# Optimization experiments

Measured on AMD Instinct MI355X. Metric: run time of the kernel, lower is better.

Reference implementation:

```python
import jax, jax.numpy as jnp
import numpy as np

N_NODES = 100000
N_EDGES = 1600000
HIDDEN = 128
N_REL = 8


def setup_inputs() -> dict:
    key = jax.random.key(0)
    ks = jax.random.split(key, 12)
    s = 1.0 / np.sqrt(HIDDEN)
    inp = {
        "node_idx": jnp.arange(N_NODES, dtype=jnp.int32),
        "edge_index": jax.random.randint(ks[0], (2, N_EDGES), 0, N_NODES, dtype=jnp.int32),
        "edge_type": jax.random.randint(ks[1], (N_EDGES,), 0, N_REL, dtype=jnp.int32),
        "embedding": jax.random.normal(ks[2], (N_NODES, HIDDEN), jnp.float32),
        "W_rel_0": jax.random.normal(ks[3], (N_REL, HIDDEN, HIDDEN), jnp.float32) * s,
        "W_root_0": jax.random.normal(ks[4], (HIDDEN, HIDDEN), jnp.float32) * s,
        "b_0": jnp.zeros((HIDDEN,), jnp.float32),
        "W_rel_1": jax.random.normal(ks[5], (N_REL, HIDDEN, HIDDEN), jnp.float32) * s,
        "W_root_1": jax.random.normal(ks[6], (HIDDEN, HIDDEN), jnp.float32) * s,
        "b_1": jnp.zeros((HIDDEN,), jnp.float32),
    }
    return inp


def _rgcn_conv(x, src, dst, et, W_rel, W_root, b):
    # PyG RGCNConv: out_i = x_i @ W_root + b + sum_r mean_{j in N_r(i)} x_j @ W_r
    n = x.shape[0]
    r = W_rel.shape[0]
    # Transform all nodes by all relations once (R small), then gather per edge.
    x_all = jnp.einsum('nd,rdf->rnf', x, W_rel)          # [R, N, d]
    msg = x_all[et, src]                                  # [E, d]
    # per-(relation, dst) mean normalization
    seg = et * n + dst                                    # [E]
    deg = jax.ops.segment_sum(jnp.ones(et.shape, jnp.float32), seg, num_segments=r * n)
    norm = 1.0 / jnp.maximum(deg[seg], 1.0)               # [E]
    agg = jax.ops.segment_sum(msg * norm[:, None], dst, num_segments=n)  # [N, d]
    return agg + x @ W_root + b


def reference(node_idx, edge_index, edge_type, embedding,
              W_rel_0, W_root_0, b_0, W_rel_1, W_root_1, b_1):
    src, dst = edge_index[0], edge_index[1]
    x = embedding[node_idx]
    x = jax.nn.relu(_rgcn_conv(x, src, dst, edge_type, W_rel_0, W_root_0, b_0))
    x = jax.nn.relu(_rgcn_conv(x, src, dst, edge_type, W_rel_1, W_root_1, b_1))
    return x
```

## Files before the change

### kernel.cpp

```cpp
#include <hip/hip_runtime.h>
#include <hip/hip_bf16.h>

typedef short bf16x8 __attribute__((ext_vector_type(8)));
typedef float f32x4 __attribute__((ext_vector_type(4)));

constexpr int NN = 100000;
constexpr int NE = 1600000;
constexpr int HH = 128;
constexpr int NR = 8;
constexpr int NBIN = 782;
constexpr int CAPB = 6144;

__device__ __forceinline__ unsigned short f2bf(float f) {
    unsigned b = __float_as_uint(f);
    b += 0x7fffu + ((b >> 16) & 1u);
    return (unsigned short)(b >> 16);
}

__global__ void convertWX(const float* __restrict__ Wr0, const float* __restrict__ Wq0,
                          const float* __restrict__ Wr1, const float* __restrict__ Wq1,
                          unsigned short* __restrict__ Wt,
                          const int* __restrict__ node_idx,
                          const float* __restrict__ emb,
                          unsigned* __restrict__ xb32) {
    if (blockIdx.x < 1152) {
        int o = blockIdx.x * 256 + threadIdx.x;
        int L = o / 147456;
        int rem = o - L * 147456;
        int s = rem >> 14;
        int p = rem & 16383;
        int f = p >> 7;
        int d = p & 127;
        const float* Wq = L ? Wq1 : Wq0;
        const float* Wr = L ? Wr1 : Wr0;
        float v = (s == 0) ? Wq[d * 128 + f] : Wr[((s - 1) * 128 + d) * 128 + f];
        Wt[o] = f2bf(v);
    } else {
        int i = (blockIdx.x - 1152) * 256 + threadIdx.x;
        if (i >= NN * 64) return;
        int n = i >> 6, dp = i & 63;
        int row = node_idx[n];
        float2 v = *((const float2*)(emb + (size_t)row * HH) + dp);
        xb32[(size_t)n * 64 + dp] = (unsigned)f2bf(v.x) | ((unsigned)f2bf(v.y) << 16);
    }
}

__global__ __launch_bounds__(256) void binCount(const int* __restrict__ edst,
                                                unsigned* __restrict__ binCounts) {
    __shared__ unsigned hist[NBIN];
    for (int i = threadIdx.x; i < NBIN; i += 256) hist[i] = 0;
    __syncthreads();
    int stride = gridDim.x * 256;
    for (int e = blockIdx.x * 256 + threadIdx.x; e < NE; e += stride)
        atomicAdd(&hist[((unsigned)edst[e]) >> 7], 1u);
    __syncthreads();
    for (int i = threadIdx.x; i < NBIN; i += 256)
        if (hist[i]) atomicAdd(&binCounts[i], hist[i]);
}

__global__ void binScan(const unsigned* __restrict__ binCounts,
                        unsigned* __restrict__ binStarts,
                        unsigned* __restrict__ binCursor) {
    __shared__ unsigned sh[1024];
    int tid = threadIdx.x;
    unsigned v = (tid < NBIN) ? binCounts[tid] : 0u;
    sh[tid] = v;
    __syncthreads();
    for (int ofs = 1; ofs < 1024; ofs <<= 1) {
        unsigned t = (tid >= ofs) ? sh[tid - ofs] : 0u;
        __syncthreads();
        sh[tid] += t;
        __syncthreads();
    }
    if (tid < NBIN) {
        unsigned s = sh[tid] - v;
        binStarts[tid] = s;
        binCursor[tid] = s;
    }
    if (tid == 0) binStarts[NBIN] = NE;
}

__global__ __launch_bounds__(256) void binScatter(
        const int* __restrict__ esrc, const int* __restrict__ edst,
        const int* __restrict__ etype, unsigned* __restrict__ binCursor,
        unsigned* __restrict__ binned) {
    __shared__ unsigned hist[NBIN];
    __shared__ unsigned cur[NBIN];
    for (int i = threadIdx.x; i < NBIN; i += 256) hist[i] = 0;
    __syncthreads();
    int per = (NE + gridDim.x - 1) / gridDim.x;
    int lo = blockIdx.x * per;
    int hi = lo + per; if (hi > NE) hi = NE;
    for (int e = lo + threadIdx.x; e < hi; e += 256)
        atomicAdd(&hist[((unsigned)edst[e]) >> 7], 1u);
    __syncthreads();
    for (int i = threadIdx.x; i < NBIN; i += 256) {
        unsigned c = hist[i];
        cur[i] = c ? atomicAdd(&binCursor[i], c) : 0u;
    }
    __syncthreads();
    for (int e = lo + threadIdx.x; e < hi; e += 256) {
        unsigned d = (unsigned)edst[e];
        unsigned b = d >> 7;
        unsigned pos = atomicAdd(&cur[b], 1u);
        binned[pos] = (unsigned)esrc[e] | (((unsigned)etype[e]) << 17) |
                      ((d & 127u) << 20);
    }
}

__global__ __launch_bounds__(256) void binSort(
        const unsigned* __restrict__ binStarts, const unsigned* __restrict__ binned,
        unsigned* __restrict__ epk, unsigned* __restrict__ starts) {
    __shared__ unsigned hist[1024];
    __shared__ unsigned scn[1024];
    __shared__ unsigned cnts[1024];
    __shared__ unsigned part[256];
    __shared__ unsigned buf[CAPB];
    __shared__ unsigned outb[CAPB];
    int bin = blockIdx.x;
    int tid = threadIdx.x;
    unsigned base = binStarts[bin];
    int cnt = (int)(binStarts[bin + 1] - base);

    for (int i = tid; i < 1024; i += 256) hist[i] = 0;
    __syncthreads();
    for (int i = tid; i < cnt; i += 256) {
        unsigned p = binned[base + i];
        if (i < CAPB) buf[i] = p;
        atomicAdd(&hist[(p >> 17) & 0x3ffu], 1u);
    }
    __syncthreads();
    unsigned h4[4], tsum = 0;
#pragma unroll
    for (int j = 0; j < 4; ++j) { h4[j] = hist[tid * 4 + j]; tsum += h4[j]; }
    part[tid] = tsum;
    __syncthreads();
    for (int ofs = 1; ofs < 256; ofs <<= 1) {
        unsigned t = (tid >= ofs) ? part[tid - ofs] : 0u;
        __syncthreads();
        part[tid] += t;
        __syncthreads();
    }
    unsigned run = part[tid] - tsum;
#pragma unroll
    for (int j = 0; j < 4; ++j) { scn[tid * 4 + j] = run; run += h4[j]; }
    __syncthreads();
    for (int i = tid; i < 1024; i += 256) {
        starts[(size_t)bin * 1024 + i] = base + scn[i];
        cnts[i] = hist[i];
        hist[i] = scn[i];
    }
    __syncthreads();
    if (cnt <= CAPB) {
        for (int i = tid; i < cnt; i += 256) {
            unsigned p = buf[i];
            unsigned key = (p >> 17) & 0x3ffu;
            unsigned pos = atomicAdd(&hist[key], 1u);
            unsigned deg = cnts[key]; if (deg > 4095u) deg = 4095u;
            outb[pos] = ((p & 0x1ffffu) << 3) | (key & 7u) | (deg << 20);
        }
        __syncthreads();
        for (int i = tid; i < cnt; i += 256) epk[base + i] = outb[i];
    } else {
        for (int i = tid; i < cnt; i += 256) {
            unsigned p = binned[base + i];
            unsigned key = (p >> 17) & 0x3ffu;
            unsigned pos = atomicAdd(&hist[key], 1u);
            unsigned deg = cnts[key]; if (deg > 4095u) deg = 4095u;
            epk[base + pos] = ((p & 0x1ffffu) << 3) | (key & 7u) | (deg << 20);
        }
    }
}

__global__ __launch_bounds__(256) void bigGemm(const unsigned short* x,
                                               const unsigned short* __restrict__ Wt,
                                               unsigned* __restrict__ y32,
                                               unsigned* root32) {
    constexpr int LDA = 136;
    __shared__ __align__(16) unsigned short A_lds[64 * LDA];
    __shared__ __align__(16) unsigned short B_lds[128 * LDA];

    int tid = threadIdx.x;
    int wid = tid >> 6, lane = tid & 63;
    int quad = lane >> 4, l16 = lane & 15;
    int wr = wid >> 1, wc = wid & 1;
    int m0 = blockIdx.x * 64;
    int chunk = tid & 15, rip = tid >> 4;

#pragma unroll
    for (int p = 0; p < 4; ++p) {
        int r = p * 16 + rip;
        int node = m0 + r;
        node = node < NN ? node : NN - 1;
        uint4 v = *((const uint4*)(x + (size_t)node * HH) + chunk);
        *(uint4*)(&A_lds[r * LDA + chunk * 8]) = v;
    }

    for (int s = 0; s < 9; ++s) {
        __syncthreads();
#pragma unroll
        for (int p = 0; p < 8; ++p) {
            int r = p * 16 + rip;
            uint4 v = *((const uint4*)(Wt + s * 16384 + r * 128) + chunk);
            *(uint4*)(&B_lds[r * LDA + chunk * 8]) = v;
        }
        __syncthreads();

        f32x4 acc[2][4];
#pragma unroll
        for (int nt = 0; nt < 2; ++nt)
#pragma unroll
            for (int ft = 0; ft < 4; ++ft) acc[nt][ft] = (f32x4){0.f, 0.f, 0.f, 0.f};

#pragma unroll
        for (int kt = 0; kt < 4; ++kt) {
            int ko = kt * 32 + quad * 8;
            bf16x8 aW[4], bx[2];
#pragma unroll
            for (int ft = 0; ft < 4; ++ft)
                aW[ft] = *(const bf16x8*)(&B_lds[(wc * 64 + ft * 16 + l16) * LDA + ko]);
#pragma unroll
            for (int nt = 0; nt < 2; ++nt)
                bx[nt] = *(const bf16x8*)(&A_lds[(wr * 32 + nt * 16 + l16) * LDA + ko]);
#pragma unroll
            for (int nt = 0; nt < 2; ++nt)
#pragma unroll
                for (int ft = 0; ft < 4; ++ft)
                    acc[nt][ft] = __builtin_amdgcn_mfma_f32_16x16x32_bf16(
                        aW[ft], bx[nt], acc[nt][ft], 0, 0, 0);
        }
#pragma unroll
        for (int nt = 0; nt < 2; ++nt) {
            int node = m0 + wr * 32 + nt * 16 + l16;
            if (node < NN) {
                unsigned* dst = (s == 0) ? (root32 + (size_t)node * 64)
                                         : (y32 + ((size_t)node * 8 + (s - 1)) * 64);
#pragma unroll
                for (int ft = 0; ft < 4; ++ft) {
                    int f0 = wc * 64 + ft * 16 + quad * 4;
                    unsigned d0, d1;
                    asm("v_cvt_pk_bf16_f32 %0, %1, %2"
                        : "=v"(d0) : "v"(acc[nt][ft][0]), "v"(acc[nt][ft][1]));
                    asm("v_cvt_pk_bf16_f32 %0, %1, %2"
                        : "=v"(d1) : "v"(acc[nt][ft][2]), "v"(acc[nt][ft][3]));
                    *(uint2*)(dst + (f0 >> 1)) = make_uint2(d0, d1);
                }
            }
        }
    }
}

__global__ __launch_bounds__(256) void scatterAgg(
        const unsigned* __restrict__ starts, const unsigned* __restrict__ epk,
        const unsigned* __restrict__ y32, const unsigned* root32,
        const float* __restrict__ bias,
        float* __restrict__ outF, unsigned* outB) {
    int node = blockIdx.x * 4 + (threadIdx.x >> 6);
    if (node >= NN) return;
    int lane = threadIdx.x & 63;

    unsigned s0 = starts[(size_t)node * 8];
    unsigned s1 = starts[(size_t)node * 8 + 8];
    int cnt = (int)__builtin_amdgcn_readfirstlane((int)(s1 - s0));

    float ax = 0.f, ay = 0.f;
    for (int c0 = 0; c0 < cnt; c0 += 64) {
        unsigned myE = s0 + (unsigned)c0 + (unsigned)lane;
        unsigned pk = (myE < s1) ? epk[myE] : 0u;
        float nrm = __builtin_amdgcn_rcpf((float)(pk >> 20));
        int cend = cnt - c0;
        if (cend > 64) cend = 64;
        for (int base = 0; base < cend; base += 8) {
            int m = cend - base;
            if (m > 8) m = 8;
            int bix = base << 2;
            unsigned pj[8], qj[8];
            float nj[8];
#pragma unroll
            for (int j = 0; j < 8; ++j) {
                pj[j] = (unsigned)__builtin_amdgcn_ds_bpermute(bix + (j << 2), (int)pk);
                nj[j] = __uint_as_float(
                    (unsigned)__builtin_amdgcn_ds_bpermute(bix + (j << 2),
                                                           __float_as_int(nrm)));
            }
#pragma unroll
            for (int j = 0; j < 8; ++j)
                if (j < m) qj[j] = y32[((pj[j] & 0xFFFFFu) << 6) + (unsigned)lane];
#pragma unroll
            for (int j = 0; j < 8; ++j) {
                if (j < m) {
                    float lo = __uint_as_float(qj[j] << 16);
                    float hi = __uint_as_float(qj[j] & 0xffff0000u);
                    ax += lo * nj[j];
                    ay += hi * nj[j];
                }
            }
        }
    }

    unsigned r = root32[(size_t)node * 64 + lane];
    float2 bv = ((const float2*)bias)[lane];
    float ox = ax + __uint_as_float(r << 16) + bv.x;
    float oy = ay + __uint_as_float(r & 0xffff0000u) + bv.y;
    ox = ox > 0.f ? ox : 0.f;
    oy = oy > 0.f ? oy : 0.f;
    if (outF) {
        *(float2*)(outF + (size_t)node * HH + lane * 2) = make_float2(ox, oy);
    } else {
        outB[(size_t)node * 64 + lane] =
            (unsigned)f2bf(ox) | ((unsigned)f2bf(oy) << 16);
    }
}

extern "C" void kernel_launch(void* const* d_in, const int* in_sizes, int n_in,
                              void* d_out, int out_size, void* d_ws, size_t ws_size,
                              hipStream_t stream) {
    const int* node_idx = (const int*)d_in[0];
    const int* eidx     = (const int*)d_in[1];
    const int* etype    = (const int*)d_in[2];
    const float* emb    = (const float*)d_in[3];
    const float* Wr0    = (const float*)d_in[4];
    const float* Wq0    = (const float*)d_in[5];
    const float* b0     = (const float*)d_in[6];
    const float* Wr1    = (const float*)d_in[7];
    const float* Wq1    = (const float*)d_in[8];
    const float* b1     = (const float*)d_in[9];
    const int* esrc = eidx;
    const int* edst = eidx + NE;

    char* ws = (char*)d_ws;
    size_t off = 0;
    auto alloc = [&](size_t bytes) -> void* {
        void* p = ws + off;
        off = (off + bytes + 255) & ~(size_t)255;
        return p;
    };
    unsigned* binCounts = (unsigned*)alloc((size_t)NBIN * 4);
    unsigned* binStarts = (unsigned*)alloc((size_t)(NBIN + 1) * 4);
    unsigned* binCursor = (unsigned*)alloc((size_t)NBIN * 4);
    unsigned* starts    = (unsigned*)alloc((size_t)NBIN * 1024 * 4);
    unsigned* epk       = (unsigned*)alloc((size_t)NE * 4);
    unsigned* xb32      = (unsigned*)alloc((size_t)NN * 64 * 4);
    unsigned* y32       = (unsigned*)alloc((size_t)NN * 8 * 64 * 4);
    unsigned short* Wt  = (unsigned short*)alloc((size_t)2 * 9 * 16384 * 2);
    unsigned* binned = y32;
    (void)ws_size; (void)n_in; (void)in_sizes; (void)out_size;

    hipMemsetAsync(binCounts, 0, (size_t)NBIN * 4, stream);
    convertWX<<<1152 + (NN * 64 + 255) / 256, 256, 0, stream>>>(
        Wr0, Wq0, Wr1, Wq1, Wt, node_idx, emb, xb32);
    binCount<<<256, 256, 0, stream>>>(edst, binCounts);
    binScan<<<1, 1024, 0, stream>>>(binCounts, binStarts, binCursor);
    binScatter<<<128, 256, 0, stream>>>(esrc, edst, etype, binCursor, binned);
    binSort<<<NBIN, 256, 0, stream>>>(binStarts, binned, epk, starts);

    int nblk = (NN + 63) / 64;
    bigGemm<<<nblk, 256, 0, stream>>>((const unsigned short*)xb32, Wt, y32, xb32);
    scatterAgg<<<(NN + 3) / 4, 256, 0, stream>>>(starts, epk, y32, xb32, b0,
                                                 nullptr, xb32);
    bigGemm<<<nblk, 256, 0, stream>>>((const unsigned short*)xb32, Wt + 147456,
                                      y32, xb32);
    scatterAgg<<<(NN + 3) / 4, 256, 0, stream>>>(starts, epk, y32, xb32, b1,
                                                 (float*)d_out, nullptr);
}
```

Before: 552.9 us.

## Load GEMM operands directly into registers, dropping LDS staging

The bigGemm kernel no longer stages the node tile and weight tiles through shared memory. Each wave loads its x fragments into registers once and reloads weight fragments per relation straight from global memory (relying on cache), which removes the LDS copies and the two barriers per stage. Launch bounds now request 3 blocks per CU. In exchange, register pressure rises and weight reads become redundant across waves and blocks, served by L1/L2 rather than LDS.

```diff
diff --git a/kernel.cpp b/kernel.cpp
--- a/kernel.cpp
+++ b/kernel.cpp
@@ -172,39 +172,36 @@
     }
 }
 
-__global__ __launch_bounds__(256) void bigGemm(const unsigned short* x,
-                                               const unsigned short* __restrict__ Wt,
-                                               unsigned* __restrict__ y32,
-                                               unsigned* root32) {
-    constexpr int LDA = 136;
-    __shared__ __align__(16) unsigned short A_lds[64 * LDA];
-    __shared__ __align__(16) unsigned short B_lds[128 * LDA];
-
+__global__ __launch_bounds__(256, 3) void bigGemm(const unsigned short* x,
+                                                  const unsigned short* __restrict__ Wt,
+                                                  unsigned* __restrict__ y32,
+                                                  unsigned* root32) {
     int tid = threadIdx.x;
     int wid = tid >> 6, lane = tid & 63;
     int quad = lane >> 4, l16 = lane & 15;
     int wr = wid >> 1, wc = wid & 1;
     int m0 = blockIdx.x * 64;
-    int chunk = tid & 15, rip = tid >> 4;
-
-#pragma unroll
-    for (int p = 0; p < 4; ++p) {
-        int r = p * 16 + rip;
-        int node = m0 + r;
+
+    bf16x8 ax[2][4];
+#pragma unroll
+    for (int nt = 0; nt < 2; ++nt) {
+        int node = m0 + wr * 32 + nt * 16 + l16;
         node = node < NN ? node : NN - 1;
-        uint4 v = *((const uint4*)(x + (size_t)node * HH) + chunk);
-        *(uint4*)(&A_lds[r * LDA + chunk * 8]) = v;
-    }
+        const unsigned short* rp = x + (size_t)node * HH + quad * 8;
+#pragma unroll
+        for (int kt = 0; kt < 4; ++kt)
+            ax[nt][kt] = *(const bf16x8*)(rp + kt * 32);
+    }
+    __syncthreads();
 
     for (int s = 0; s < 9; ++s) {
-        __syncthreads();
-#pragma unroll
-        for (int p = 0; p < 8; ++p) {
-            int r = p * 16 + rip;
-            uint4 v = *((const uint4*)(Wt + s * 16384 + r * 128) + chunk);
-            *(uint4*)(&B_lds[r * LDA + chunk * 8]) = v;
-        }
-        __syncthreads();
+        const unsigned short* Bb = Wt + s * 16384 + (wc * 64 + l16) * 128 + quad * 8;
+        bf16x8 bw[4][4];
+#pragma unroll
+        for (int ft = 0; ft < 4; ++ft)
+#pragma unroll
+            for (int kt = 0; kt < 4; ++kt)
+                bw[ft][kt] = *(const bf16x8*)(Bb + ft * (16 * 128) + kt * 32);
 
         f32x4 acc[2][4];
 #pragma unroll
@@ -213,22 +210,14 @@
             for (int ft = 0; ft < 4; ++ft) acc[nt][ft] = (f32x4){0.f, 0.f, 0.f, 0.f};
 
 #pragma unroll
-        for (int kt = 0; kt < 4; ++kt) {
-            int ko = kt * 32 + quad * 8;
-            bf16x8 aW[4], bx[2];
-#pragma unroll
-            for (int ft = 0; ft < 4; ++ft)
-                aW[ft] = *(const bf16x8*)(&B_lds[(wc * 64 + ft * 16 + l16) * LDA + ko]);
-#pragma unroll
-            for (int nt = 0; nt < 2; ++nt)
-                bx[nt] = *(const bf16x8*)(&A_lds[(wr * 32 + nt * 16 + l16) * LDA + ko]);
+        for (int kt = 0; kt < 4; ++kt)
 #pragma unroll
             for (int nt = 0; nt < 2; ++nt)
 #pragma unroll
                 for (int ft = 0; ft < 4; ++ft)
                     acc[nt][ft] = __builtin_amdgcn_mfma_f32_16x16x32_bf16(
-                        aW[ft], bx[nt], acc[nt][ft], 0, 0, 0);
-        }
+                        bw[ft][kt], ax[nt][kt], acc[nt][ft], 0, 0, 0);
+
 #pragma unroll
         for (int nt = 0; nt < 2; ++nt) {
             int node = m0 + wr * 32 + nt * 16 + l16;
```

Measured after the change: 657.1 us. 1.19x slower.
